# Optimization experiments

Hardware: AMD Instinct MI355X
Metric: run time of the kernel (lower is better)

The kernel has to match this reference:

```python
import jax, jax.numpy as jnp
import numpy as np

B, T, D, E, F, K = 1, 8192, 1024, 8, 4096, 2
CAP_FACTOR = 1.25
AUX_COEFF = 0.01


def setup_inputs() -> dict:
    key = jax.random.key(0)
    k0, k1, k2, k3, k4 = jax.random.split(key, 5)
    x = jax.random.normal(k0, (B, T, D), dtype=jnp.float32)
    Wr = jax.random.normal(k1, (E, D), dtype=jnp.float32) * 0.01  # router, std=0.01 per init
    s = 0.02
    Wg = jax.random.normal(k2, (E, F, D), dtype=jnp.float32) * s  # gate_proj per expert
    Wu = jax.random.normal(k3, (E, F, D), dtype=jnp.float32) * s  # up_proj per expert
    Wd = jax.random.normal(k4, (E, D, F), dtype=jnp.float32) * s  # down_proj per expert
    return {"x": x, "Wr": Wr, "Wg": Wg, "Wu": Wu, "Wd": Wd}


def reference(x, Wr, Wg, Wu, Wd):
    b, t, d = x.shape
    N = b * t
    capacity = max(int(t * K * CAP_FACTOR / E), 1)  # static, matches compute_capacity
    x_flat = x.reshape(N, d)

    # --- router ---
    logits = x_flat @ Wr.T                              # (N, E)
    probs = jax.nn.softmax(logits, axis=-1)
    topw_raw, topi = jax.lax.top_k(probs, K)            # (N, K)
    topw = topw_raw / (topw_raw.sum(-1, keepdims=True) + 1e-9)

    # --- dispatch order: slot-major (slot 0 over all tokens, then slot 1, ...) ---
    flat_e = topi.T.reshape(-1)                         # (K*N,) expert id per assignment
    flat_w = topw.T.reshape(-1)                         # (K*N,)
    tok = jnp.tile(jnp.arange(N), K)                    # (K*N,) token id per assignment

    oh = jax.nn.one_hot(flat_e, E, dtype=jnp.int32)     # (K*N, E)
    rank = (jnp.cumsum(oh, axis=0) - oh)[jnp.arange(K * N), flat_e]  # arrival rank per expert
    accepted = rank < capacity                          # dispatch_mask (slot-major flat)
    pos = jnp.where(accepted, rank, 0)
    dest = flat_e * capacity + pos                      # slot in flattened capacity buffer
    acc_f = accepted.astype(x.dtype)[:, None]

    # scatter tokens into capacity buffers (dropped tokens add zeros)
    buf = jnp.zeros((E * capacity, d), x.dtype).at[dest].add(x_flat[tok] * acc_f)
    expert_in = buf.reshape(E, capacity, d)

    # --- per-expert SwiGLU FFN (batched grouped GEMM) ---
    gate = jax.nn.silu(jnp.einsum('ecd,efd->ecf', expert_in, Wg))
    up = jnp.einsum('ecd,efd->ecf', expert_in, Wu)
    expert_out = jnp.einsum('ecf,edf->ecd', gate * up, Wd).reshape(E * capacity, d)

    # --- weighted combine back to token positions ---
    contrib = flat_w[:, None] * acc_f * expert_out[dest]
    out_flat = jnp.zeros((N, d), x.dtype).at[tok].add(contrib)
    output = out_flat.reshape(b, t, d)

    # --- load-balance aux loss ---
    counts = jnp.zeros(E, x.dtype).at[flat_e].add(accepted.astype(x.dtype))
    total = jnp.maximum(accepted.sum().astype(x.dtype), 1.0)
    f_i = counts / total
    P_i = probs.mean(0)
    aux_loss = AUX_COEFF * E * jnp.sum(f_i * P_i)
    return output, aux_loss
```

## Files before the change

kernel.cpp:

```cpp
#include <hip/hip_runtime.h>
#include <hip/hip_bf16.h>

#define N_TOK 8192
#define DIM   1024
#define NEXP  8
#define FF    4096
#define CAP   2560
#define NASSIGN (N_TOK * 2)

typedef __bf16 bf16;
typedef __bf16 bf16x8 __attribute__((ext_vector_type(8)));
typedef __bf16 bf16x4v __attribute__((ext_vector_type(4)));
typedef float  f32x4  __attribute__((ext_vector_type(4)));

__device__ __forceinline__ void gl2lds16(const bf16* g, bf16* l) {
    __builtin_amdgcn_global_load_lds(
        (const __attribute__((address_space(1))) unsigned int*)g,
        (__attribute__((address_space(3))) unsigned int*)l,
        16, 0, 0);
}

template <int NT, int AST, int BST, int BG1, int BG2>
__device__ __forceinline__ void gemm256_core(
    const bf16* __restrict__ pA, const bf16* __restrict__ pB,
    bf16* As, bf16* Bs, f32x4 acc[8][4], int wave, int lane)
{
    const int wm = wave >> 2, wn = wave & 3;
    const int r16 = lane & 15, c16 = lane >> 4;
    const int wbase = wave * 8 * 64;

#define AOFF(g) ((size_t)(g) * 64 * AST)
#define BOFF(g) ((size_t)(((g) & 1) * BG1 + ((g) >> 1) * BG2) * BST)
#define SA(g, kt) gl2lds16(pA + AOFF(g) + (size_t)(kt) * 64, \
                           &As[((kt) & 1) * (256 * 64) + (g) * (64 * 64) + wbase])
#define SB(g, kt) gl2lds16(pB + BOFF(g) + (size_t)(kt) * 64, \
                           &Bs[((kt) & 1) * (256 * 64) + (g) * (64 * 64) + wbase])

    SA(0, 0); SA(2, 0); SB(0, 0); SB(1, 0);
    SA(1, 0); SA(3, 0); SB(2, 0); SB(3, 0);
    SA(0, 1); SA(2, 1); SB(0, 1); SB(1, 1);
    asm volatile("s_waitcnt vmcnt(4)" ::: "memory");
    __builtin_amdgcn_sched_barrier(0);
    __builtin_amdgcn_s_barrier();
    __builtin_amdgcn_sched_barrier(0);

    bf16x8 af[4][2], bfr[2][2];

#define DS_A(mh)                                                           \
    _Pragma("unroll")                                                      \
    for (int mm = 0; mm < 4; ++mm) {                                       \
        _Pragma("unroll")                                                  \
        for (int kk = 0; kk < 2; ++kk) {                                   \
            int row = wm * 128 + (mh) * 64 + mm * 16 + r16;                \
            int phys = (kk * 4 + c16) ^ (row & 7);                         \
            af[mm][kk] = *(const bf16x8*)&Asb[row * 64 + phys * 8];        \
        } }
#define DS_B(nh)                                                           \
    _Pragma("unroll")                                                      \
    for (int np = 0; np < 2; ++np) {                                       \
        _Pragma("unroll")                                                  \
        for (int kk = 0; kk < 2; ++kk) {                                   \
            int rl = (nh) * 128 + wn * 32 + np * 16 + r16;                 \
            int phys = (kk * 4 + c16) ^ (rl & 7);                          \
            bfr[np][kk] = *(const bf16x8*)&Bsb[rl * 64 + phys * 8];        \
        } }
#define PH_IN                                                              \
    __builtin_amdgcn_sched_barrier(0);                                     \
    __builtin_amdgcn_s_barrier();                                          \
    asm volatile("s_waitcnt lgkmcnt(0)" ::: "memory");                     \
    __builtin_amdgcn_sched_barrier(0);
#define MFMA16(mh, nh)                                                     \
    __builtin_amdgcn_s_setprio(1);                                         \
    _Pragma("unroll")                                                      \
    for (int mm = 0; mm < 4; ++mm)                                         \
        _Pragma("unroll")                                                  \
        for (int np = 0; np < 2; ++np)                                     \
            _Pragma("unroll")                                              \
            for (int kk = 0; kk < 2; ++kk)                                 \
                acc[(mh) * 4 + mm][(nh) * 2 + np] =                        \
                    __builtin_amdgcn_mfma_f32_16x16x32_bf16(               \
                        af[mm][kk], bfr[np][kk],                           \
                        acc[(mh) * 4 + mm][(nh) * 2 + np], 0, 0, 0);       \
    __builtin_amdgcn_s_setprio(0);
#define PH_OUT                                                             \
    __builtin_amdgcn_sched_barrier(0);                                     \
    __builtin_amdgcn_s_barrier();                                          \
    __builtin_amdgcn_sched_barrier(0);

#define TILE(kt, S1, S2, VMC) {                                            \
    const bf16* Asb = &As[((kt) & 1) * (256 * 64)];                        \
    const bf16* Bsb = &Bs[((kt) & 1) * (256 * 64)];                        \
    DS_A(0) DS_B(0)                                                        \
    if (S1) { SA(1, (kt) + 1); SA(3, (kt) + 1); }                          \
    PH_IN MFMA16(0, 0) PH_OUT                                              \
    DS_B(1)                                                                \
    if (S1) { SB(2, (kt) + 1); SB(3, (kt) + 1); }                          \
    PH_IN MFMA16(0, 1) PH_OUT                                              \
    DS_A(1) DS_B(0)                                                        \
    if (S2) { SA(0, (kt) + 2); SA(2, (kt) + 2); }                          \
    PH_IN MFMA16(1, 0) PH_OUT                                              \
    DS_B(1)                                                                \
    if (S2) { SB(0, (kt) + 2); SB(1, (kt) + 2); }                          \
    if ((VMC) == 4) { asm volatile("s_waitcnt vmcnt(4)" ::: "memory"); }   \
    else if ((VMC) == 0) { asm volatile("s_waitcnt vmcnt(0)" ::: "memory"); } \
    PH_IN MFMA16(1, 1) PH_OUT }

    for (int kt = 0; kt < NT - 2; ++kt) TILE(kt, 1, 1, 4);
    TILE(NT - 2, 1, 0, 0);
    TILE(NT - 1, 0, 0, -1);

#undef AOFF
#undef BOFF
#undef SA
#undef SB
#undef DS_A
#undef DS_B
#undef PH_IN
#undef MFMA16
#undef PH_OUT
#undef TILE
}

__global__ __launch_bounds__(256) void cvt_bf16_kernel(const float* __restrict__ in,
                                                       bf16* __restrict__ out, int n) {
    int stride = gridDim.x * blockDim.x * 8;
    for (int i = (blockIdx.x * blockDim.x + threadIdx.x) * 8; i < n; i += stride) {
        float4 a = *(const float4*)(in + i);
        float4 b = *(const float4*)(in + i + 4);
        bf16x8 o;
        o[0] = (bf16)a.x; o[1] = (bf16)a.y; o[2] = (bf16)a.z; o[3] = (bf16)a.w;
        o[4] = (bf16)b.x; o[5] = (bf16)b.y; o[6] = (bf16)b.z; o[7] = (bf16)b.w;
        *(bf16x8*)(out + i) = o;
    }
}

__global__ __launch_bounds__(256) void router_kernel(const float* __restrict__ x,
                                                     const float* __restrict__ Wr,
                                                     float* __restrict__ probs,
                                                     int* __restrict__ topi,
                                                     float* __restrict__ topw) {
    int wave = threadIdx.x >> 6;
    int lane = threadIdx.x & 63;
    int t = blockIdx.x * 4 + wave;
    const float* xr = x + (size_t)t * DIM;

    double acc[NEXP];
#pragma unroll
    for (int e = 0; e < NEXP; ++e) acc[e] = 0.0;
    for (int i = lane; i < DIM; i += 64) {
        double xv = (double)xr[i];
#pragma unroll
        for (int e = 0; e < NEXP; ++e) acc[e] += xv * (double)Wr[e * DIM + i];
    }
#pragma unroll
    for (int e = 0; e < NEXP; ++e) {
        double v = acc[e];
        for (int off = 32; off > 0; off >>= 1) v += __shfl_down(v, off, 64);
        acc[e] = v;
    }
    if (lane == 0) {
        double mx = acc[0];
        for (int e = 1; e < NEXP; ++e) if (acc[e] > mx) mx = acc[e];
        double p[NEXP], s = 0.0;
        for (int e = 0; e < NEXP; ++e) { p[e] = exp(acc[e] - mx); s += p[e]; }
        float pf[NEXP];
        for (int e = 0; e < NEXP; ++e) { pf[e] = (float)(p[e] / s); probs[t * NEXP + e] = pf[e]; }
        int e1 = 0;
        for (int e = 1; e < NEXP; ++e) if (acc[e] > acc[e1]) e1 = e;
        int e2 = -1;
        for (int e = 0; e < NEXP; ++e) {
            if (e == e1) continue;
            if (e2 < 0 || acc[e] > acc[e2]) e2 = e;
        }
        float w1 = pf[e1], w2 = pf[e2];
        float inv = 1.0f / (w1 + w2 + 1e-9f);
        topi[t * 2 + 0] = e1; topi[t * 2 + 1] = e2;
        topw[t * 2 + 0] = w1 * inv; topw[t * 2 + 1] = w2 * inv;
    }
}

__global__ __launch_bounds__(64) void rank_kernel(const int* __restrict__ topi,
                                                  int* __restrict__ dest,
                                                  int* __restrict__ accf,
                                                  int* __restrict__ counts) {
    int e = blockIdx.x;
    int lane = threadIdx.x;
    const int per = NASSIGN / 64;
    int base = lane * per;
    int cnt = 0;
    for (int i = 0; i < per; ++i) {
        int j = base + i;
        int t = j & (N_TOK - 1), s = j >> 13;
        if (topi[t * 2 + s] == e) cnt++;
    }
    int sum = cnt;
    for (int off = 1; off < 64; off <<= 1) {
        int v = __shfl_up(sum, off, 64);
        if (lane >= off) sum += v;
    }
    int r = sum - cnt;
    int total = __shfl(sum, 63, 64);
    for (int i = 0; i < per; ++i) {
        int j = base + i;
        int t = j & (N_TOK - 1), s = j >> 13;
        if (topi[t * 2 + s] == e) {
            int acc = (r < CAP) ? 1 : 0;
            dest[j] = e * CAP + (acc ? r : 0);
            accf[j] = acc;
            r++;
        }
    }
    if (lane == 63) counts[e] = (total < CAP) ? total : CAP;
}

__global__ __launch_bounds__(256) void gather_kernel(const float* __restrict__ x,
                                                     const int* __restrict__ dest,
                                                     const int* __restrict__ accf,
                                                     bf16* __restrict__ Xe) {
    int j = blockIdx.x;
    if (!accf[j]) return;
    int t = j & (N_TOK - 1);
    int d0 = threadIdx.x * 4;
    float4 v = *(const float4*)(x + (size_t)t * DIM + d0);
    union { bf16 h[4]; uint2 u; } tmp;
    tmp.h[0] = (bf16)v.x; tmp.h[1] = (bf16)v.y; tmp.h[2] = (bf16)v.z; tmp.h[3] = (bf16)v.w;
    *(uint2*)(Xe + (size_t)dest[j] * DIM + d0) = tmp.u;
}

__global__ __launch_bounds__(512, 2) void gateup_kernel(const bf16* __restrict__ Xe,
                                                        const bf16* __restrict__ Wg,
                                                        const bf16* __restrict__ Wu,
                                                        bf16* __restrict__ hbuf) {
    const int e = blockIdx.z;
    const int m0 = blockIdx.x * 256;
    const int n0f = blockIdx.y * 128;
    const int tid = threadIdx.x, lane = tid & 63, wave = tid >> 6;
    const int wm = wave >> 2, wn = wave & 3;
    const int r16 = lane & 15, c16 = lane >> 4;

    __shared__ bf16 As[2 * 256 * 64];
    __shared__ bf16 Bs[2 * 256 * 64];

    const int l   = wave * 8 + (lane >> 3);
    const int csw = ((lane & 7) ^ (lane >> 3)) * 8;
    const bf16* pA = Xe + (size_t)e * CAP * DIM + (size_t)(m0 + l) * DIM + csw;
    const int T = (l >> 4) & 1, wnl = l >> 5, r16l = l & 15;
    const bf16* pB = (T ? Wu : Wg) + (size_t)e * FF * DIM
                   + (size_t)(n0f + wnl * 32 + r16l) * DIM + csw;

    f32x4 acc[8][4] = {};
    gemm256_core<DIM / 64, DIM, DIM, 64, 16>(pA, pB, As, Bs, acc, wave, lane);

    bf16* hp = hbuf + (size_t)e * CAP * FF;
#pragma unroll
    for (int m = 0; m < 8; ++m)
#pragma unroll
        for (int cg = 0; cg < 2; ++cg)
#pragma unroll
            for (int j = 0; j < 4; ++j) {
                float g = acc[m][cg * 2 + 0][j];
                float u = acc[m][cg * 2 + 1][j];
                float h = (g / (1.f + __expf(-g))) * u;
                int gr = m0 + wm * 128 + m * 16 + c16 * 4 + j;
                int gc = n0f + wn * 32 + cg * 16 + r16;
                hp[(size_t)gr * FF + gc] = (bf16)h;
            }
}

__global__ __launch_bounds__(512, 2) void down_kernel(const bf16* __restrict__ hbuf,
                                                      const bf16* __restrict__ Wd,
                                                      bf16* __restrict__ eo) {
    const int e  = blockIdx.z >> 1;
    const int kh = blockIdx.z & 1;
    const int m0 = blockIdx.x * 256;
    const int n0 = blockIdx.y * 256;
    const int tid = threadIdx.x, lane = tid & 63, wave = tid >> 6;
    const int wm = wave >> 2, wn = wave & 3;
    const int r16 = lane & 15, c16 = lane >> 4;

    __shared__ bf16 As[2 * 256 * 64];
    __shared__ bf16 Bs[2 * 256 * 64];

    const int l   = wave * 8 + (lane >> 3);
    const int csw = ((lane & 7) ^ (lane >> 3)) * 8;
    const bf16* pA = hbuf + (size_t)e * CAP * FF + (size_t)(m0 + l) * FF
                   + kh * (FF / 2) + csw;
    const int nlow = (l >> 4) & 1, wnl = l >> 5, r16l = l & 15;
    const bf16* pB = Wd + (size_t)e * DIM * FF
                   + (size_t)(n0 + wnl * 64 + nlow * 16 + r16l) * FF
                   + kh * (FF / 2) + csw;

    f32x4 acc[8][4] = {};
    gemm256_core<FF / 128, FF, FF, 128, 32>(pA, pB, As, Bs, acc, wave, lane);

    bf16* op = eo + (size_t)kh * NEXP * CAP * DIM + (size_t)e * CAP * DIM;
#pragma unroll
    for (int m = 0; m < 8; ++m)
#pragma unroll
        for (int n = 0; n < 4; ++n)
#pragma unroll
            for (int j = 0; j < 4; ++j) {
                int gr = m0 + wm * 128 + m * 16 + c16 * 4 + j;
                int gc = n0 + wn * 64 + n * 16 + r16;
                op[(size_t)gr * DIM + gc] = (bf16)acc[m][n][j];
            }
}

__global__ __launch_bounds__(256) void combine_kernel(const bf16* __restrict__ eo,
                                                      const int* __restrict__ dest,
                                                      const int* __restrict__ accf,
                                                      const float* __restrict__ topw,
                                                      float* __restrict__ out) {
    int t = blockIdx.x;
    float w0 = accf[t] ? topw[t * 2 + 0] : 0.f;
    float w1 = accf[N_TOK + t] ? topw[t * 2 + 1] : 0.f;
    size_t off1 = (size_t)NEXP * CAP * DIM;
    const bf16* a0 = eo + (size_t)dest[t] * DIM;
    const bf16* b0 = eo + (size_t)dest[N_TOK + t] * DIM;
    int d = threadIdx.x * 4;
    bf16x4v a00 = *(const bf16x4v*)(a0 + d);
    bf16x4v a01 = *(const bf16x4v*)(a0 + off1 + d);
    bf16x4v b00 = *(const bf16x4v*)(b0 + d);
    bf16x4v b01 = *(const bf16x4v*)(b0 + off1 + d);
    float4 o;
    o.x = w0 * ((float)a00[0] + (float)a01[0]) + w1 * ((float)b00[0] + (float)b01[0]);
    o.y = w0 * ((float)a00[1] + (float)a01[1]) + w1 * ((float)b00[1] + (float)b01[1]);
    o.z = w0 * ((float)a00[2] + (float)a01[2]) + w1 * ((float)b00[2] + (float)b01[2]);
    o.w = w0 * ((float)a00[3] + (float)a01[3]) + w1 * ((float)b00[3] + (float)b01[3]);
    *(float4*)(out + (size_t)t * DIM + d) = o;
}

__global__ __launch_bounds__(256) void aux_kernel(const float* __restrict__ probs,
                                                  const int* __restrict__ counts,
                                                  float* __restrict__ out_aux) {
    __shared__ float sm[256][NEXP];
    float loc[NEXP];
#pragma unroll
    for (int e = 0; e < NEXP; ++e) loc[e] = 0.f;
    for (int t = threadIdx.x; t < N_TOK; t += 256)
#pragma unroll
        for (int e = 0; e < NEXP; ++e) loc[e] += probs[t * NEXP + e];
#pragma unroll
    for (int e = 0; e < NEXP; ++e) sm[threadIdx.x][e] = loc[e];
    __syncthreads();
    for (int s = 128; s > 0; s >>= 1) {
        if (threadIdx.x < s)
#pragma unroll
            for (int e = 0; e < NEXP; ++e) sm[threadIdx.x][e] += sm[threadIdx.x + s][e];
        __syncthreads();
    }
    if (threadIdx.x == 0) {
        int tot = 0;
        for (int e = 0; e < NEXP; ++e) tot += counts[e];
        float totf = tot > 0 ? (float)tot : 1.f;
        float aux = 0.f;
        for (int e = 0; e < NEXP; ++e)
            aux += ((float)counts[e] / totf) * (sm[0][e] / (float)N_TOK);
        out_aux[0] = 0.01f * (float)NEXP * aux;
    }
}

extern "C" void kernel_launch(void* const* d_in, const int* in_sizes, int n_in,
                              void* d_out, int out_size, void* d_ws, size_t ws_size,
                              hipStream_t stream) {
    const float* x  = (const float*)d_in[0];
    const float* Wr = (const float*)d_in[1];
    const float* Wg = (const float*)d_in[2];
    const float* Wu = (const float*)d_in[3];
    const float* Wd = (const float*)d_in[4];
    float* out = (float*)d_out;

    char* ws = (char*)d_ws;
    size_t off = 0;
    auto alloc = [&](size_t bytes) -> void* {
        void* p = ws + off;
        off += (bytes + 255) & ~(size_t)255;
        return p;
    };
    const size_t NW = (size_t)NEXP * FF * DIM;
    bf16*  Wg_bf = (bf16*)alloc(NW * sizeof(bf16));
    bf16*  Wu_bf = (bf16*)alloc(NW * sizeof(bf16));
    bf16*  Wd_bf = (bf16*)alloc(NW * sizeof(bf16));
    bf16*  Xe    = (bf16*)alloc((size_t)NEXP * CAP * DIM * sizeof(bf16));
    bf16*  hbuf  = (bf16*)alloc((size_t)NEXP * CAP * FF * sizeof(bf16));
    bf16*  eo    = (bf16*)alloc((size_t)2 * NEXP * CAP * DIM * sizeof(bf16));
    float* probs = (float*)alloc((size_t)N_TOK * NEXP * sizeof(float));
    int*   topi  = (int*)alloc((size_t)N_TOK * 2 * sizeof(int));
    float* topw  = (float*)alloc((size_t)N_TOK * 2 * sizeof(float));
    int*   dst   = (int*)alloc((size_t)NASSIGN * sizeof(int));
    int*   accf  = (int*)alloc((size_t)NASSIGN * sizeof(int));
    int*   cnts  = (int*)alloc(NEXP * sizeof(int));

    cvt_bf16_kernel<<<2048, 256, 0, stream>>>(Wg, Wg_bf, (int)NW);
    cvt_bf16_kernel<<<2048, 256, 0, stream>>>(Wu, Wu_bf, (int)NW);
    cvt_bf16_kernel<<<2048, 256, 0, stream>>>(Wd, Wd_bf, (int)NW);
    router_kernel<<<N_TOK / 4, 256, 0, stream>>>(x, Wr, probs, topi, topw);
    rank_kernel<<<NEXP, 64, 0, stream>>>(topi, dst, accf, cnts);
    gather_kernel<<<NASSIGN, 256, 0, stream>>>(x, dst, accf, Xe);
    gateup_kernel<<<dim3(CAP / 256, FF / 128, NEXP), 512, 0, stream>>>(Xe, Wg_bf, Wu_bf, hbuf);
    down_kernel<<<dim3(CAP / 256, DIM / 256, NEXP * 2), 512, 0, stream>>>(hbuf, Wd_bf, eo);
    combine_kernel<<<N_TOK, 256, 0, stream>>>(eo, dst, accf, topw, out);
    aux_kernel<<<1, 256, 0, stream>>>(probs, cnts, out + (size_t)N_TOK * DIM);
}
```

Measured before the change: 896.5 us.

## Replace 4-phase interleaved GEMM pipeline with simple 2-phase loop and XCD-aware block remap

Swaps the hand-interleaved GEMM main loop, which split each k-tile into four MFMA phases with partial prefetches and fine-grained vmcnt waits, for a simpler loop. The new loop prefetches the whole next tile, runs all MFMAs for the current tile, then does a full vmcnt(0) wait and barrier. Both GEMM kernels also remap linear block IDs so that blocks landing on the same XCD (lin & 7) share an expert, aiming for better L2 reuse of that expert's weights. The simpler pipeline has fewer barriers but overlaps loads with compute more coarsely, and the remap adds some index arithmetic.

```diff
diff --git a/kernel.cpp b/kernel.cpp
--- a/kernel.cpp
+++ b/kernel.cpp
@@ -21,104 +21,82 @@
 }
 
 template <int NT, int AST, int BST, int BG1, int BG2>
-__device__ __forceinline__ void gemm256_core(
+__device__ __forceinline__ void gemm256_2ph(
     const bf16* __restrict__ pA, const bf16* __restrict__ pB,
-    bf16* As, bf16* Bs, f32x4 acc[8][4], int wave, int lane)
+    f32x4 acc[8][4], int wave, int lane)
 {
+    __shared__ bf16 As[2 * 256 * 64];
+    __shared__ bf16 Bs[2 * 256 * 64];
+
     const int wm = wave >> 2, wn = wave & 3;
     const int r16 = lane & 15, c16 = lane >> 4;
     const int wbase = wave * 8 * 64;
 
-#define AOFF(g) ((size_t)(g) * 64 * AST)
-#define BOFF(g) ((size_t)(((g) & 1) * BG1 + ((g) >> 1) * BG2) * BST)
-#define SA(g, kt) gl2lds16(pA + AOFF(g) + (size_t)(kt) * 64, \
-                           &As[((kt) & 1) * (256 * 64) + (g) * (64 * 64) + wbase])
-#define SB(g, kt) gl2lds16(pB + BOFF(g) + (size_t)(kt) * 64, \
-                           &Bs[((kt) & 1) * (256 * 64) + (g) * (64 * 64) + wbase])
-
-    SA(0, 0); SA(2, 0); SB(0, 0); SB(1, 0);
-    SA(1, 0); SA(3, 0); SB(2, 0); SB(3, 0);
-    SA(0, 1); SA(2, 1); SB(0, 1); SB(1, 1);
-    asm volatile("s_waitcnt vmcnt(4)" ::: "memory");
+    auto STAGE = [&](int kt) {
+        const int b = kt & 1;
+        const bf16* a  = pA + (size_t)kt * 64;
+        const bf16* bb = pB + (size_t)kt * 64;
+#pragma unroll
+        for (int g = 0; g < 4; ++g)
+            gl2lds16(a + (size_t)g * 64 * AST,
+                     &As[b * (256 * 64) + g * (64 * 64) + wbase]);
+#pragma unroll
+        for (int g = 0; g < 4; ++g)
+            gl2lds16(bb + (size_t)((g & 1) * BG1 + (g >> 1) * BG2) * BST,
+                     &Bs[b * (256 * 64) + g * (64 * 64) + wbase]);
+    };
+
+    STAGE(0);
+    asm volatile("s_waitcnt vmcnt(0)" ::: "memory");
     __builtin_amdgcn_sched_barrier(0);
     __builtin_amdgcn_s_barrier();
     __builtin_amdgcn_sched_barrier(0);
 
-    bf16x8 af[4][2], bfr[2][2];
-
-#define DS_A(mh)                                                           \
-    _Pragma("unroll")                                                      \
-    for (int mm = 0; mm < 4; ++mm) {                                       \
-        _Pragma("unroll")                                                  \
-        for (int kk = 0; kk < 2; ++kk) {                                   \
-            int row = wm * 128 + (mh) * 64 + mm * 16 + r16;                \
-            int phys = (kk * 4 + c16) ^ (row & 7);                         \
-            af[mm][kk] = *(const bf16x8*)&Asb[row * 64 + phys * 8];        \
-        } }
-#define DS_B(nh)                                                           \
-    _Pragma("unroll")                                                      \
-    for (int np = 0; np < 2; ++np) {                                       \
-        _Pragma("unroll")                                                  \
-        for (int kk = 0; kk < 2; ++kk) {                                   \
-            int rl = (nh) * 128 + wn * 32 + np * 16 + r16;                 \
-            int phys = (kk * 4 + c16) ^ (rl & 7);                          \
-            bfr[np][kk] = *(const bf16x8*)&Bsb[rl * 64 + phys * 8];        \
-        } }
-#define PH_IN                                                              \
-    __builtin_amdgcn_sched_barrier(0);                                     \
-    __builtin_amdgcn_s_barrier();                                          \
-    asm volatile("s_waitcnt lgkmcnt(0)" ::: "memory");                     \
-    __builtin_amdgcn_sched_barrier(0);
-#define MFMA16(mh, nh)                                                     \
-    __builtin_amdgcn_s_setprio(1);                                         \
-    _Pragma("unroll")                                                      \
-    for (int mm = 0; mm < 4; ++mm)                                         \
-        _Pragma("unroll")                                                  \
-        for (int np = 0; np < 2; ++np)                                     \
-            _Pragma("unroll")                                              \
-            for (int kk = 0; kk < 2; ++kk)                                 \
-                acc[(mh) * 4 + mm][(nh) * 2 + np] =                        \
-                    __builtin_amdgcn_mfma_f32_16x16x32_bf16(               \
-                        af[mm][kk], bfr[np][kk],                           \
-                        acc[(mh) * 4 + mm][(nh) * 2 + np], 0, 0, 0);       \
-    __builtin_amdgcn_s_setprio(0);
-#define PH_OUT                                                             \
-    __builtin_amdgcn_sched_barrier(0);                                     \
-    __builtin_amdgcn_s_barrier();                                          \
-    __builtin_amdgcn_sched_barrier(0);
-
-#define TILE(kt, S1, S2, VMC) {                                            \
-    const bf16* Asb = &As[((kt) & 1) * (256 * 64)];                        \
-    const bf16* Bsb = &Bs[((kt) & 1) * (256 * 64)];                        \
-    DS_A(0) DS_B(0)                                                        \
-    if (S1) { SA(1, (kt) + 1); SA(3, (kt) + 1); }                          \
-    PH_IN MFMA16(0, 0) PH_OUT                                              \
-    DS_B(1)                                                                \
-    if (S1) { SB(2, (kt) + 1); SB(3, (kt) + 1); }                          \
-    PH_IN MFMA16(0, 1) PH_OUT                                              \
-    DS_A(1) DS_B(0)                                                        \
-    if (S2) { SA(0, (kt) + 2); SA(2, (kt) + 2); }                          \
-    PH_IN MFMA16(1, 0) PH_OUT                                              \
-    DS_B(1)                                                                \
-    if (S2) { SB(0, (kt) + 2); SB(1, (kt) + 2); }                          \
-    if ((VMC) == 4) { asm volatile("s_waitcnt vmcnt(4)" ::: "memory"); }   \
-    else if ((VMC) == 0) { asm volatile("s_waitcnt vmcnt(0)" ::: "memory"); } \
-    PH_IN MFMA16(1, 1) PH_OUT }
-
-    for (int kt = 0; kt < NT - 2; ++kt) TILE(kt, 1, 1, 4);
-    TILE(NT - 2, 1, 0, 0);
-    TILE(NT - 1, 0, 0, -1);
-
-#undef AOFF
-#undef BOFF
-#undef SA
-#undef SB
-#undef DS_A
-#undef DS_B
-#undef PH_IN
-#undef MFMA16
-#undef PH_OUT
-#undef TILE
+    for (int kt = 0; kt < NT; ++kt) {
+        if (kt + 1 < NT) STAGE(kt + 1);
+        const bf16* Asb = &As[(kt & 1) * (256 * 64)];
+        const bf16* Bsb = &Bs[(kt & 1) * (256 * 64)];
+
+        bf16x8 bfr[4][2];
+#pragma unroll
+        for (int nh = 0; nh < 2; ++nh)
+#pragma unroll
+            for (int np = 0; np < 2; ++np)
+#pragma unroll
+                for (int kk = 0; kk < 2; ++kk) {
+                    int rl = nh * 128 + wn * 32 + np * 16 + r16;
+                    int phys = (kk * 4 + c16) ^ (rl & 7);
+                    bfr[nh * 2 + np][kk] = *(const bf16x8*)&Bsb[rl * 64 + phys * 8];
+                }
+#pragma unroll
+        for (int mh = 0; mh < 2; ++mh) {
+            bf16x8 af[4][2];
+#pragma unroll
+            for (int mm = 0; mm < 4; ++mm)
+#pragma unroll
+                for (int kk = 0; kk < 2; ++kk) {
+                    int row = wm * 128 + mh * 64 + mm * 16 + r16;
+                    int phys = (kk * 4 + c16) ^ (row & 7);
+                    af[mm][kk] = *(const bf16x8*)&Asb[row * 64 + phys * 8];
+                }
+            __builtin_amdgcn_s_setprio(1);
+#pragma unroll
+            for (int mm = 0; mm < 4; ++mm)
+#pragma unroll
+                for (int nf = 0; nf < 4; ++nf)
+#pragma unroll
+                    for (int kk = 0; kk < 2; ++kk)
+                        acc[mh * 4 + mm][nf] =
+                            __builtin_amdgcn_mfma_f32_16x16x32_bf16(
+                                af[mm][kk], bfr[nf][kk], acc[mh * 4 + mm][nf], 0, 0, 0);
+            __builtin_amdgcn_s_setprio(0);
+        }
+
+        asm volatile("s_waitcnt vmcnt(0)" ::: "memory");
+        __builtin_amdgcn_sched_barrier(0);
+        __builtin_amdgcn_s_barrier();
+        __builtin_amdgcn_sched_barrier(0);
+    }
 }
 
 __global__ __launch_bounds__(256) void cvt_bf16_kernel(const float* __restrict__ in,
@@ -231,15 +209,14 @@
                                                         const bf16* __restrict__ Wg,
                                                         const bf16* __restrict__ Wu,
                                                         bf16* __restrict__ hbuf) {
-    const int e = blockIdx.z;
-    const int m0 = blockIdx.x * 256;
-    const int n0f = blockIdx.y * 128;
+    const int lin = blockIdx.x + 10 * (blockIdx.y + 32 * blockIdx.z);
+    const int e   = lin & 7;
+    const int rem = lin >> 3;
+    const int m0  = (rem % 10) * 256;
+    const int n0f = (rem / 10) * 128;
     const int tid = threadIdx.x, lane = tid & 63, wave = tid >> 6;
     const int wm = wave >> 2, wn = wave & 3;
     const int r16 = lane & 15, c16 = lane >> 4;
-
-    __shared__ bf16 As[2 * 256 * 64];
-    __shared__ bf16 Bs[2 * 256 * 64];
 
     const int l   = wave * 8 + (lane >> 3);
     const int csw = ((lane & 7) ^ (lane >> 3)) * 8;
@@ -249,7 +226,7 @@
                    + (size_t)(n0f + wnl * 32 + r16l) * DIM + csw;
 
     f32x4 acc[8][4] = {};
-    gemm256_core<DIM / 64, DIM, DIM, 64, 16>(pA, pB, As, Bs, acc, wave, lane);
+    gemm256_2ph<DIM / 64, DIM, DIM, 64, 16>(pA, pB, acc, wave, lane);
 
     bf16* hp = hbuf + (size_t)e * CAP * FF;
 #pragma unroll
@@ -270,16 +247,16 @@
 __global__ __launch_bounds__(512, 2) void down_kernel(const bf16* __restrict__ hbuf,
                                                       const bf16* __restrict__ Wd,
                                                       bf16* __restrict__ eo) {
-    const int e  = blockIdx.z >> 1;
-    const int kh = blockIdx.z & 1;
-    const int m0 = blockIdx.x * 256;
-    const int n0 = blockIdx.y * 256;
+    const int lin = blockIdx.x + 10 * (blockIdx.y + 4 * blockIdx.z);
+    const int xcd = lin & 7, pos = lin >> 3;
+    const int zc  = xcd * 2 + pos / 40;
+    const int e = zc >> 1, kh = zc & 1;
+    const int rem40 = pos % 40;
+    const int m0 = (rem40 % 10) * 256;
+    const int n0 = (rem40 / 10) * 256;
     const int tid = threadIdx.x, lane = tid & 63, wave = tid >> 6;
     const int wm = wave >> 2, wn = wave & 3;
     const int r16 = lane & 15, c16 = lane >> 4;
-
-    __shared__ bf16 As[2 * 256 * 64];
-    __shared__ bf16 Bs[2 * 256 * 64];
 
     const int l   = wave * 8 + (lane >> 3);
     const int csw = ((lane & 7) ^ (lane >> 3)) * 8;
@@ -291,7 +268,7 @@
                    + kh * (FF / 2) + csw;
 
     f32x4 acc[8][4] = {};
-    gemm256_core<FF / 128, FF, FF, 128, 32>(pA, pB, As, Bs, acc, wave, lane);
+    gemm256_2ph<FF / 128, FF, FF, 128, 32>(pA, pB, acc, wave, lane);
 
     bf16* op = eo + (size_t)kh * NEXP * CAP * DIM + (size_t)e * CAP * DIM;
 #pragma unroll
```

Measured after the change: 853.0 us. -4.9%, faster.
